# Kernel optimization log

Hardware: AMD Instinct MI355X
Metric: run time of the kernel (lower is better)

## Reference

```python
import jax, jax.numpy as jnp
import numpy as np

V = 32000   # vocab
E = 512     # hidden_size (d_model)
NH = 8      # num_heads
DH = E // NH
NL = 2      # num_layers
FF = 2048   # TransformerDecoderLayer default dim_feedforward
MAXLEN = 24 # cfg.max_length -> gen_len (no target given)
S, B = 48, 8
TRANS = 14
INIT = TRANS - 2            # tgt = transform[1:-1]
LF = INIT + MAXLEN - 1      # final tgt length after the loop
EPS = 1e-5
NEG = -1e9


def pos_encoding(length, d):
    pos = np.arange(length, dtype=np.float32)[:, None]
    div = np.exp(-np.log(10000.0) * np.arange(0, d, 2, dtype=np.float32) / d)
    pe = np.zeros((length, d), dtype=np.float32)
    pe[:, 0::2] = np.sin(pos * div)
    pe[:, 1::2] = np.cos(pos * div)
    return jnp.asarray(pe)


def setup_inputs() -> dict:
    key = jax.random.key(0)
    ks = jax.random.split(key, 12)
    s = 0.02
    return {
        "enc_outputs": jax.random.normal(ks[0], (S, B, E), jnp.float32),
        "transform": jax.random.randint(ks[1], (TRANS, B), 0, V),
        "tf_ratio": 0,
        "emb_table": jax.random.normal(ks[2], (V, E), jnp.float32) * s,
        "sa_w": jax.random.normal(ks[3], (NL, 3 * E, E), jnp.float32) * s,
        "sa_b": jnp.zeros((NL, 3 * E), jnp.float32),
        "sa_ow": jax.random.normal(ks[4], (NL, E, E), jnp.float32) * s,
        "sa_ob": jnp.zeros((NL, E), jnp.float32),
        "ca_w": jax.random.normal(ks[5], (NL, 3 * E, E), jnp.float32) * s,
        "ca_b": jnp.zeros((NL, 3 * E), jnp.float32),
        "ca_ow": jax.random.normal(ks[6], (NL, E, E), jnp.float32) * s,
        "ca_ob": jnp.zeros((NL, E), jnp.float32),
        "ff1_w": jax.random.normal(ks[7], (NL, FF, E), jnp.float32) * s,
        "ff1_b": jnp.zeros((NL, FF), jnp.float32),
        "ff2_w": jax.random.normal(ks[8], (NL, E, FF), jnp.float32) * s,
        "ff2_b": jnp.zeros((NL, E), jnp.float32),
        "ln_g": jnp.ones((NL, 3, E), jnp.float32),
        "ln_b": jnp.zeros((NL, 3, E), jnp.float32),
        "out_w": jax.random.normal(ks[9], (V, E), jnp.float32) * s,
        "out_b": jnp.zeros((V,), jnp.float32),
    }


def _ln(x, g, b):
    m = jnp.mean(x, -1, keepdims=True)
    v = jnp.mean((x - m) ** 2, -1, keepdims=True)
    return (x - m) * jax.lax.rsqrt(v + EPS) * g + b


def _mha(q_in, kv_in, w, b, ow, ob, mask):
    # q_in [Lq,B,E], kv_in [Lk,B,E]; PyTorch packed in_proj [3E,E]
    wq, wk, wv = jnp.split(w, 3, 0)
    bq, bk, bv = jnp.split(b, 3, 0)
    proj = lambda x, wm, bm: (x @ wm.T + bm).reshape(x.shape[0], x.shape[1], NH, DH)
    q, k, v = proj(q_in, wq, bq), proj(kv_in, wk, bk), proj(kv_in, wv, bv)
    sc = jnp.einsum('qbhd,kbhd->bhqk', q, k) / np.sqrt(DH).astype(np.float32)
    if mask is not None:
        sc = sc + mask
    a = jax.nn.softmax(sc, -1)
    o = jnp.einsum('bhqk,kbhd->qbhd', a, v).reshape(q_in.shape[0], q_in.shape[1], E)
    return o @ ow.T + ob


def _decoder(x, mem, mask, p):
    # post-norm TransformerDecoderLayer: self-attn -> cross-attn -> relu FFN
    for l in range(NL):
        x = _ln(x + _mha(x, x, p['sa_w'][l], p['sa_b'][l], p['sa_ow'][l], p['sa_ob'][l], mask),
                p['ln_g'][l, 0], p['ln_b'][l, 0])
        x = _ln(x + _mha(x, mem, p['ca_w'][l], p['ca_b'][l], p['ca_ow'][l], p['ca_ob'][l], None),
                p['ln_g'][l, 1], p['ln_b'][l, 1])
        h = jax.nn.relu(x @ p['ff1_w'][l].T + p['ff1_b'][l]) @ p['ff2_w'][l].T + p['ff2_b'][l]
        x = _ln(x + h, p['ln_g'][l, 2], p['ln_b'][l, 2])
    return x


def reference(enc_outputs, transform, tf_ratio, emb_table, sa_w, sa_b, sa_ow, sa_ob,
              ca_w, ca_b, ca_ow, ca_ob, ff1_w, ff1_b, ff2_w, ff2_b, ln_g, ln_b,
              out_w, out_b):
    # tf_ratio == 0 -> no teacher forcing; gen_len = max_length (no target attr)
    p = dict(sa_w=sa_w, sa_b=sa_b, sa_ow=sa_ow, sa_ob=sa_ob, ca_w=ca_w, ca_b=ca_b,
             ca_ow=ca_ow, ca_ob=ca_ob, ff1_w=ff1_w, ff1_b=ff1_b, ff2_w=ff2_w,
             ff2_b=ff2_b, ln_g=ln_g, ln_b=ln_b)
    pe = pos_encoding(MAXLEN, E)
    # causal mask over the fixed-size buffer; padded (future) slots cannot
    # influence valid positions, so full-buffer passes == torch prefix passes.
    mask = jnp.where(jnp.tril(jnp.ones((LF, LF), bool)), 0.0, NEG)
    tgt0 = emb_table[transform[1:-1]] + pe[:INIT][:, None, :]   # [INIT,B,E]
    buf = jnp.zeros((LF, B, E), jnp.float32).at[:INIT].set(tgt0)

    def step(buf, i):
        h = _decoder(buf, enc_outputs, mask, p)
        pos = INIT - 1 + i                        # last valid position
        pred = jnp.argmax(h[pos] @ out_w.T + out_b, axis=-1)   # [B]
        # torch re-embeds the single predicted token -> PE position 0
        emb = emb_table[pred] + pe[0]
        return buf.at[pos + 1].set(emb), None

    buf, _ = jax.lax.scan(step, buf, jnp.arange(MAXLEN - 1))
    h = _decoder(buf, enc_outputs, mask, p)       # final loop iteration's pass
    return h @ out_w.T + out_b                    # dec_outputs [LF,B,V]
```

## Files before the change

kernel.cpp:

```cpp
#include <hip/hip_runtime.h>
#include <hip/hip_bf16.h>
#include <math.h>

#define V    32000
#define E    512
#define NH   8
#define DH   64
#define NL   2
#define FF   2048
#define MAXLEN 24
#define S    48
#define B    8
#define TRANS 14
#define INIT 12
#define LF   35

#define NB   256
#define NT   1024

typedef float f4 __attribute__((ext_vector_type(4)));

__device__ inline float wsum(float v) {
#pragma unroll
  for (int off = 32; off; off >>= 1) v += __shfl_xor(v, off);
  return v;
}
__device__ inline float wmax(float v) {
#pragma unroll
  for (int off = 32; off; off >>= 1) v = fmaxf(v, __shfl_xor(v, off));
  return v;
}

__device__ inline void stc(float* p, float v) {
  __hip_atomic_store(p, v, __ATOMIC_RELAXED, __HIP_MEMORY_SCOPE_AGENT);
}
__device__ inline void stc8(float* p, float x, float y) {
  union { unsigned long long u; float f[2]; } c; c.f[0] = x; c.f[1] = y;
  __hip_atomic_store((unsigned long long*)p, c.u, __ATOMIC_RELAXED, __HIP_MEMORY_SCOPE_AGENT);
}
__device__ inline int ldci(const int* p) {
  return __hip_atomic_load(p, __ATOMIC_RELAXED, __HIP_MEMORY_SCOPE_AGENT);
}
__device__ inline void stci(int* p, int v) {
  __hip_atomic_store(p, v, __ATOMIC_RELAXED, __HIP_MEMORY_SCOPE_AGENT);
}

#define CMB(v, idx, ov, oi) do { if ((ov) > (v) || ((ov) == (v) && (oi) < (idx))) { (v) = (ov); (idx) = (oi); } } while (0)


__global__ void embed_init_k(const int* __restrict__ transform, const float* __restrict__ emb,
                             float* __restrict__ xbuf) {
  int t = blockIdx.x;
  int pos = t >> 3, b = t & 7;
  int tok = transform[(1 + pos) * B + b];
  for (int d = threadIdx.x; d < E; d += blockDim.x) {
    double div = exp(-log(10000.0) * (double)(d & ~1) / (double)E);
    double ang = (double)pos * div;
    float pe = (d & 1) ? (float)cos(ang) : (float)sin(ang);
    xbuf[(size_t)t * E + d] = emb[(size_t)tok * E + d] + pe;
  }
}

template <int K>
__global__ __launch_bounds__(256) void gemm_k(
    const float* __restrict__ x, const float* __restrict__ W, const float* __restrict__ bias,
    int ntok, int nout, int route, int relu,
    float* __restrict__ out0, float* __restrict__ out1, float* __restrict__ out2) {
  constexpr int K4 = K / 4;
  constexpr int J  = K / 256;
  __shared__ float4 xt[8][K4];
  const int tid = threadIdx.x;
  const int lane = tid & 63;
  const int o = blockIdx.x * 4 + (tid >> 6);

  float4 wr[J];
  if (o < nout) {
    const float4* Wr = (const float4*)(W + (size_t)o * K);
#pragma unroll
    for (int j = 0; j < J; ++j) wr[j] = Wr[lane + 64 * j];
  }

  const int ng = ntok >> 3;
  for (int g = 0; g < ng; ++g) {
    if (g) __syncthreads();
    const float4* xg = (const float4*)(x + (size_t)g * 8 * K);
    float4* xf = &xt[0][0];
    for (int i = tid; i < 8 * K4; i += 256) xf[i] = xg[i];
    __syncthreads();
    if (o < nout) {
      float acc[8] = {0, 0, 0, 0, 0, 0, 0, 0};
#pragma unroll
      for (int j = 0; j < J; ++j) {
        float4 w = wr[j];
#pragma unroll
        for (int tt = 0; tt < 8; ++tt) {
          float4 xv = xt[tt][lane + 64 * j];
          acc[tt] += w.x * xv.x + w.y * xv.y + w.z * xv.z + w.w * xv.w;
        }
      }
#pragma unroll
      for (int tt = 0; tt < 8; ++tt) acc[tt] = wsum(acc[tt]);
      if (lane == 0) {
        float bo = bias[o];
#pragma unroll
        for (int tt = 0; tt < 8; ++tt) {
          float v = acc[tt] + bo;
          if (relu) v = fmaxf(v, 0.f);
          int t = g * 8 + tt;
          if (route == 0) {
            out0[(size_t)t * nout + o] = v;
          } else if (route == 1) {
            if (o < E) out0[(size_t)t * E + o] = v;
            else if (o < 2 * E) out1[(size_t)t * E + (o - E)] = v;
            else out2[(size_t)t * E + (o - 2 * E)] = v;
          } else {
            if (o < E) out0[(size_t)t * E + o] = v;
            else out1[(size_t)t * E + (o - E)] = v;
          }
        }
      }
    }
  }
}

__global__ __launch_bounds__(256) void attn_k(
    const float* __restrict__ q, const float* __restrict__ Kc, const float* __restrict__ Vc,
    float* __restrict__ outp, int p0, int nq, int nk_fixed, int causal) {
  const int tid = threadIdx.x;
  const int lane = tid & 63;
  const int u = blockIdx.x * 4 + (tid >> 6);
  if (u >= nq * 64) return;
  const int qi = u >> 6;
  const int r = u & 63;
  const int b = r >> 3, h = r & 7;
  const int nk = causal ? (p0 + qi + 1) : nk_fixed;

  const size_t qoff = (size_t)(qi * B + b) * E + h * DH + lane;
  const float qv = q[qoff];

  float myscore = -INFINITY;
  for (int k = 0; k < nk; ++k) {
    float prod = qv * Kc[(size_t)(k * B + b) * E + h * DH + lane];
    prod = wsum(prod);
    if (lane == k) myscore = prod * 0.125f;
  }
  float m = wmax(myscore);
  float p = (lane < nk) ? expf(myscore - m) : 0.f;
  float denom = wsum(p);
  float a = p / denom;

  float oacc = 0.f;
  for (int k = 0; k < nk; ++k) {
    float ak = __shfl(a, k);
    oacc = fmaf(ak, Vc[(size_t)(k * B + b) * E + h * DH + lane], oacc);
  }
  outp[qoff] = oacc;
}

__global__ __launch_bounds__(256) void add_ln_k(
    const float* __restrict__ xa, const float* __restrict__ xb,
    const float* __restrict__ g, const float* __restrict__ beta,
    float* __restrict__ outp, int ntok) {
  const int tid = threadIdx.x, lane = tid & 63;
  const int t = blockIdx.x * 4 + (tid >> 6);
  if (t >= ntok) return;
  float v[8];
  float s = 0.f;
#pragma unroll
  for (int j = 0; j < 8; ++j) {
    int d = lane + 64 * j;
    v[j] = xa[(size_t)t * E + d] + xb[(size_t)t * E + d];
    s += v[j];
  }
  s = wsum(s);
  float mean = s * (1.f / 512.f);
  float d2 = 0.f;
#pragma unroll
  for (int j = 0; j < 8; ++j) { float dd = v[j] - mean; d2 += dd * dd; }
  d2 = wsum(d2);
  float inv = 1.f / sqrtf(d2 * (1.f / 512.f) + 1e-5f);
#pragma unroll
  for (int j = 0; j < 8; ++j) {
    int d = lane + 64 * j;
    outp[(size_t)t * E + d] = (v[j] - mean) * inv * g[d] + beta[d];
  }
}

#define B_QKV 0
#define B_OW  6144
#define B_CQ  8192
#define B_COW 10240
#define B_FF1 12288
#define B_FF2 20480
#define SW_TOT 28672
#define SLOTS_PER_STEP 23

__global__ __launch_bounds__(NT, 1) void decode_persist_k(
    const float* __restrict__ emb,
    const float* __restrict__ sa_w, const float* __restrict__ sa_b,
    const float* __restrict__ sa_ow, const float* __restrict__ sa_ob,
    const float* __restrict__ ca_w, const float* __restrict__ ca_b,
    const float* __restrict__ ca_ow, const float* __restrict__ ca_ob,
    const float* __restrict__ ff1_w, const float* __restrict__ ff1_b,
    const float* __restrict__ ff2_w, const float* __restrict__ ff2_b,
    const float* __restrict__ ln_g, const float* __restrict__ ln_b,
    const float* __restrict__ out_w, const float* __restrict__ out_b,
    float* __restrict__ kself, float* __restrict__ vself,
    const float* __restrict__ kcross, const float* __restrict__ vcross,
    float* __restrict__ arena, float* __restrict__ outp, int* __restrict__ bar) {
  __shared__ __align__(16) float s_w[SW_TOT];
  __shared__ __align__(16) float s_x[8 * E];
  __shared__ __align__(16) float s_raw[8 * E];
  __shared__ __align__(16) float s_q2[64];
  __shared__ __align__(16) float s_attw[64];
  __shared__ __align__(16) float s_part[4][64];
  __shared__ int   s_tok[8];
  __shared__ float s_pv[16][8];
  __shared__ int   s_pi[16][8];

  const int tid  = threadIdx.x;
  const int lane = tid & 63;
  const int wv   = tid >> 6;
  const int bid  = blockIdx.x;
  int gen = 0;

  auto slot = [&](int st, int s) -> float* {
    return arena + ((size_t)st * SLOTS_PER_STEP + s) * 4096;
  };

  auto gbar = [&]() {
    ++gen;
    __syncthreads();
    if (tid == 0)
      __hip_atomic_fetch_add(&bar[(bid & 31) * 32], 1, __ATOMIC_RELAXED, __HIP_MEMORY_SCOPE_AGENT);
    if (bid == 0 && wv == 0) {
      const int tgt = gen * 8;
      for (;;) {
        int c = (lane < 32) ? ldci(&bar[lane * 32]) : tgt;
        if (__all(c >= tgt)) break;
        __builtin_amdgcn_s_sleep(1);
      }
      if (lane == 0) stci(&bar[40 * 32], gen);
    }
    if (wv == 0) {
      while (ldci(&bar[40 * 32]) < gen) __builtin_amdgcn_s_sleep(2);
    }
    __syncthreads();
  };

  auto stage_raw = [&](const float* src) {
    const float4* s4 = (const float4*)src;
    float4* d4 = (float4*)s_raw;
    for (int k = tid; k < 1024; k += NT) d4[k] = s4[k];
    __syncthreads();
  };
  auto lnstage = [&](int lnidx) {
    if (wv < 8) {
      const float* gg = ln_g + (size_t)lnidx * E;
      const float* be = ln_b + (size_t)lnidx * E;
      float v[8]; float sum = 0.f;
#pragma unroll
      for (int j = 0; j < 8; ++j) {
        int d = lane + 64 * j;
        v[j] = s_x[wv * E + d] + s_raw[wv * E + d];
        sum += v[j];
      }
      sum = wsum(sum);
      float mean = sum * (1.f / 512.f);
      float d2 = 0.f;
#pragma unroll
      for (int j = 0; j < 8; ++j) { float dd = v[j] - mean; d2 += dd * dd; }
      d2 = wsum(d2);
      float inv = 1.f / sqrtf(d2 * (1.f / 512.f) + 1e-5f);
#pragma unroll
      for (int j = 0; j < 8; ++j) {
        int d = lane + 64 * j;
        s_x[wv * E + d] = (v[j] - mean) * inv * gg[d] + be[d];
      }
    }
    __syncthreads();
  };
  auto proj16 = [&](int wbase, const float* srcLDS, const float* biasp, float* dst) {
    int j = wv & 1, b = wv >> 1;
    int r = bid * 2 + j;
    const f4* wp = (const f4*)&s_w[wbase + j * 512];
    f4 w0 = wp[lane], w1 = wp[lane + 64];
    const f4* x4 = (const f4*)(srcLDS + b * E);
    f4 a = w0 * x4[lane] + w1 * x4[lane + 64];
    float acc = a.x + a.y + a.z + a.w;
    acc = wsum(acc);
    if (lane == 0) stc(&dst[b * E + r], acc + biasp[r]);
  };
  auto attn_stage = [&](const float* qsrc, const float* Kbase, const float* Vbase,
                        int nk, float* attdst) {
    const int b = bid >> 3, h = bid & 7;
    if (wv == 0) {
      s_q2[lane] = qsrc[b * E + h * DH + lane];
      float sc = -INFINITY;
      if (lane < nk) {
        const f4* Kr = (const f4*)(Kbase + ((size_t)lane * B + b) * E + h * DH);
        const f4* Qp = (const f4*)s_q2;
        float a0 = 0.f;
#pragma unroll
        for (int u = 0; u < 16; ++u) {
          f4 kv = Kr[u], qq = Qp[u];
          a0 += kv.x * qq.x + kv.y * qq.y + kv.z * qq.z + kv.w * qq.w;
        }
        sc = a0 * 0.125f;
      }
      float m = wmax(sc);
      float e = (lane < nk) ? expf(sc - m) : 0.f;
      float den = wsum(e);
      s_attw[lane] = e / den;
    }
    __syncthreads();
    if (wv < 4) {
      float o = 0.f;
      for (int k = wv; k < nk; k += 4)
        o = fmaf(s_attw[k], Vbase[((size_t)k * B + b) * E + h * DH + lane], o);
      s_part[wv][lane] = o;
    }
    __syncthreads();
    if (wv == 0)
      stc(&attdst[b * E + h * DH + lane],
          s_part[0][lane] + s_part[1][lane] + s_part[2][lane] + s_part[3][lane]);
  };

  {
    auto cprow = [&](const float* src, int dstf) {
      f4* d = (f4*)&s_w[dstf]; const f4* s = (const f4*)src;
      for (int k = tid; k < 128; k += NT) d[k] = s[k];
    };
    for (int l = 0; l < NL; ++l) {
      for (int j = 0; j < 6; ++j)
        cprow(sa_w + ((size_t)l * 1536 + bid * 6 + j) * E, B_QKV + (l * 6 + j) * 512);
      for (int j = 0; j < 2; ++j) {
        cprow(sa_ow + ((size_t)l * 512 + bid * 2 + j) * E, B_OW + (l * 2 + j) * 512);
        cprow(ca_w + ((size_t)l * 1536 + bid * 2 + j) * E, B_CQ + (l * 2 + j) * 512);
        cprow(ca_ow + ((size_t)l * 512 + bid * 2 + j) * E, B_COW + (l * 2 + j) * 512);
      }
      for (int j = 0; j < 8; ++j)
        cprow(ff1_w + ((size_t)l * FF + bid * 8 + j) * E, B_FF1 + (l * 8 + j) * 512);
    }
    const int lf2 = bid >> 7;
    for (int j = 0; j < 4; ++j) {
      f4* d = (f4*)&s_w[B_FF2 + j * 2048];
      const f4* s = (const f4*)(ff2_w + ((size_t)lf2 * 512 + (bid & 127) * 4 + j) * FF);
      for (int k = tid; k < 512; k += NT) d[k] = s[k];
    }
    __syncthreads();
  }

  for (int i = 0; i < MAXLEN - 1; ++i) {
    const int p = INIT + i;
    float* amax_o = slot(i, 0);

    {
      int bw = wv & 7;
      float v = -INFINITY; int ix = 0x7fffffff;
      if (i == 0) {
        const float2* row = (const float2*)(outp + ((size_t)(INIT - 1) * B + bw) * V);
        for (int jj = lane; jj < V / 2; jj += 64) {
          float2 t = row[jj];
          CMB(v, ix, t.x, 2 * jj);
          CMB(v, ix, t.y, 2 * jj + 1);
        }
      } else {
        const float2* ap = (const float2*)slot(i - 1, 0);
#pragma unroll
        for (int t = 0; t < 4; ++t) {
          int e = lane * 4 + t;
          float2 pr = ap[e * 8 + bw];
          CMB(v, ix, pr.x, (int)pr.y);
        }
      }
#pragma unroll
      for (int off = 1; off < 64; off <<= 1) {
        float ov = __shfl_xor(v, off); int oi = __shfl_xor(ix, off);
        CMB(v, ix, ov, oi);
      }
      if (lane == 0 && wv < 8) s_tok[bw] = ix;
      __syncthreads();
      int b = tid >> 7, d0 = (tid & 127) * 4;
      int tok = s_tok[b];
      float4 ev = *(const float4*)(emb + (size_t)tok * E + d0);
      s_x[b * E + d0]     = ev.x;
      s_x[b * E + d0 + 1] = ev.y + 1.0f;
      s_x[b * E + d0 + 2] = ev.z;
      s_x[b * E + d0 + 3] = ev.w + 1.0f;
      __syncthreads();
    }

    for (int l = 0; l < NL; ++l) {
      float* Lb    = slot(i, 1 + l * 11);
      float* q_s   = Lb;
      float* att_s = Lb + 4096;
      float* raw_s = Lb + 8192;
      float* q_c   = Lb + 12288;
      float* att_c = Lb + 16384;
      float* raw_c = Lb + 20480;
      float* hb    = Lb + 24576;
      float* yb    = Lb + 40960;

      if (wv < 12) {
        int j = wv >> 1, bg = (wv & 1) * 4;
        int r = bid * 6 + j, sec = r >> 9, off = r & 511;
        const f4* wp = (const f4*)&s_w[B_QKV + (l * 6 + j) * 512];
        f4 w0 = wp[lane], w1 = wp[lane + 64];
        float bias = sa_b[(size_t)l * 1536 + r];
        for (int b = bg; b < bg + 4; ++b) {
          const f4* x4 = (const f4*)&s_x[b * E];
          f4 a = w0 * x4[lane] + w1 * x4[lane + 64];
          float acc = a.x + a.y + a.z + a.w;
          acc = wsum(acc);
          if (lane == 0) {
            acc += bias;
            if (sec == 0) stc(&q_s[b * E + off], acc);
            else if (sec == 1) stc(&kself[((size_t)(l * LF + p) * B + b) * E + off], acc);
            else stc(&vself[((size_t)(l * LF + p) * B + b) * E + off], acc);
          }
        }
      }
      gbar();
      if (bid < 64)
        attn_stage(q_s, kself + (size_t)l * LF * B * E, vself + (size_t)l * LF * B * E,
                   p + 1, att_s);
      gbar();
      stage_raw(att_s);
      proj16(B_OW + l * 1024, s_raw, sa_ob + (size_t)l * E, raw_s);
      gbar();
      stage_raw(raw_s);
      lnstage(l * 3 + 0);
      proj16(B_CQ + l * 1024, s_x, ca_b + (size_t)l * 3 * E, q_c);
      gbar();
      if (bid < 64)
        attn_stage(q_c, kcross + (size_t)l * S * B * E, vcross + (size_t)l * S * B * E,
                   S, att_c);
      gbar();
      stage_raw(att_c);
      proj16(B_COW + l * 1024, s_raw, ca_ob + (size_t)l * E, raw_c);
      gbar();
      stage_raw(raw_c);
      lnstage(l * 3 + 1);
      {
        int j = wv >> 1, bg = (wv & 1) * 4;
        int r = bid * 8 + j;
        const f4* wp = (const f4*)&s_w[B_FF1 + (l * 8 + j) * 512];
        f4 w0 = wp[lane], w1 = wp[lane + 64];
        float bias = ff1_b[(size_t)l * FF + r];
        for (int b = bg; b < bg + 4; ++b) {
          const f4* x4 = (const f4*)&s_x[b * E];
          f4 a = w0 * x4[lane] + w1 * x4[lane + 64];
          float acc = a.x + a.y + a.z + a.w;
          acc = wsum(acc);
          if (lane == 0) stc(&hb[b * FF + r], fmaxf(acc + bias, 0.f));
        }
      }
      gbar();
      if ((bid >> 7) == l) {
        int b = wv >> 1, j0 = (wv & 1) * 2;
        int r0 = (bid & 127) * 4;
        const f4* h4 = (const f4*)(hb + b * FF);
        f4 hv[8];
#pragma unroll
        for (int j = 0; j < 8; ++j) hv[j] = h4[j * 64 + lane];
#pragma unroll
        for (int jr = 0; jr < 2; ++jr) {
          int rl = j0 + jr;
          const f4* wp = (const f4*)&s_w[B_FF2 + rl * 2048];
          float acc = 0.f;
#pragma unroll
          for (int j = 0; j < 8; ++j) {
            f4 w = wp[j * 64 + lane];
            acc += w.x * hv[j].x + w.y * hv[j].y + w.z * hv[j].z + w.w * hv[j].w;
          }
          acc = wsum(acc);
          if (lane == 0)
            stc(&yb[b * E + r0 + rl], acc + ff2_b[(size_t)l * 512 + r0 + rl]);
        }
      }
      gbar();
      stage_raw(yb);
      lnstage(l * 3 + 2);
    }

    {
      const int grp = lane >> 3, sub = lane & 7;
      const int idx = wv * 8 + grp;
      const bool valid = idx < 125;
      const int r = bid * 125 + idx;
      float acc[8] = {0, 0, 0, 0, 0, 0, 0, 0};
      if (valid) {
        const f4* wrow = (const f4*)(out_w + (size_t)r * E);
#pragma unroll
        for (int half = 0; half < 2; ++half) {
          f4 w8[8];
#pragma unroll
          for (int j = 0; j < 8; ++j) w8[j] = wrow[(half * 8 + j) * 8 + sub];
#pragma unroll
          for (int b = 0; b < 8; ++b) {
            const f4* x4 = (const f4*)&s_x[b * E];
            float a = 0.f;
#pragma unroll
            for (int j = 0; j < 8; ++j) {
              f4 xx = x4[(half * 8 + j) * 8 + sub];
              a += w8[j].x * xx.x + w8[j].y * xx.y + w8[j].z * xx.z + w8[j].w * xx.w;
            }
            acc[b] += a;
          }
        }
#pragma unroll
        for (int b = 0; b < 8; ++b) {
          acc[b] += __shfl_xor(acc[b], 1);
          acc[b] += __shfl_xor(acc[b], 2);
          acc[b] += __shfl_xor(acc[b], 4);
        }
        if (sub == 0) {
          float bo = out_b[r];
#pragma unroll
          for (int b = 0; b < 8; ++b) {
            acc[b] += bo;
            outp[((size_t)p * B + b) * V + r] = acc[b];
          }
        }
      }
#pragma unroll
      for (int b = 0; b < 8; ++b) {
        float v = (valid && sub == 0) ? acc[b] : -INFINITY;
        int ix = (valid && sub == 0) ? r : 0x7fffffff;
#pragma unroll
        for (int off = 1; off < 64; off <<= 1) {
          float ov = __shfl_xor(v, off); int oi = __shfl_xor(ix, off);
          CMB(v, ix, ov, oi);
        }
        if (lane == 0) { s_pv[wv][b] = v; s_pi[wv][b] = ix; }
      }
      __syncthreads();
      if (wv == 0) {
        int b = lane & 7, w2 = lane >> 3;
        float v = s_pv[w2][b]; int ix = s_pi[w2][b];
        float v2 = s_pv[w2 + 8][b]; int ix2 = s_pi[w2 + 8][b];
        CMB(v, ix, v2, ix2);
#pragma unroll
        for (int off = 8; off < 64; off <<= 1) {
          float ov = __shfl_xor(v, off); int oi = __shfl_xor(ix, off);
          CMB(v, ix, ov, oi);
        }
        if (lane < 8) stc8(&amax_o[(size_t)(bid * 8 + lane) * 2], v, (float)ix);
      }
    }
    gbar();
  }
}

extern "C" void kernel_launch(void* const* d_in, const int* in_sizes, int n_in,
                              void* d_out, int out_size, void* d_ws, size_t ws_size,
                              hipStream_t stream) {
  const float* enc       = (const float*)d_in[0];
  const int*   transform = (const int*)d_in[1];
  const float* emb       = (const float*)d_in[3];
  const float* sa_w  = (const float*)d_in[4];
  const float* sa_b  = (const float*)d_in[5];
  const float* sa_ow = (const float*)d_in[6];
  const float* sa_ob = (const float*)d_in[7];
  const float* ca_w  = (const float*)d_in[8];
  const float* ca_b  = (const float*)d_in[9];
  const float* ca_ow = (const float*)d_in[10];
  const float* ca_ob = (const float*)d_in[11];
  const float* ff1_w = (const float*)d_in[12];
  const float* ff1_b = (const float*)d_in[13];
  const float* ff2_w = (const float*)d_in[14];
  const float* ff2_b = (const float*)d_in[15];
  const float* ln_g  = (const float*)d_in[16];
  const float* ln_b  = (const float*)d_in[17];
  const float* out_w = (const float*)d_in[18];
  const float* out_b = (const float*)d_in[19];
  float* out = (float*)d_out;

  const size_t SELF_SZ  = (size_t)LF * B * E;
  const size_t CROSS_SZ = (size_t)S * B * E;
  const size_t ARENA_SZ = (size_t)(MAXLEN - 1) * SLOTS_PER_STEP * 4096;
  float* ws     = (float*)d_ws;
  float* xbuf   = ws;
  float* kself  = xbuf + (size_t)INIT * B * E;
  float* vself  = kself + NL * SELF_SZ;
  float* kcross = vself + NL * SELF_SZ;
  float* vcross = kcross + NL * CROSS_SZ;
  float* arena  = vcross + NL * CROSS_SZ;
  int*   bar    = (int*)(arena + ARENA_SZ);
  float* act1   = (float*)(bar + 64 * 32);
  float* act2   = act1 + 96 * E;
  float* act3   = act2 + 96 * E;
  float* ffb    = act3 + 96 * E;

  hipMemsetAsync(bar, 0, 64 * 32 * 4, stream);

  embed_init_k<<<INIT * B, 128, 0, stream>>>(transform, emb, xbuf);

  for (int l = 0; l < NL; ++l) {
    gemm_k<E><<<(2 * E) / 4, 256, 0, stream>>>(
        enc, ca_w + ((size_t)l * 3 * E + E) * E, ca_b + (size_t)l * 3 * E + E,
        S * B, 2 * E, 2, 0, kcross + l * CROSS_SZ, vcross + l * CROSS_SZ, nullptr);
  }

  {
    const int p0 = 0, nq = INIT, ntok = nq * B;
    const float* xin = xbuf;
    for (int l = 0; l < NL; ++l) {
      const float* x = (l == 0) ? xin : act1;
      gemm_k<E><<<(3 * E) / 4, 256, 0, stream>>>(
          x, sa_w + (size_t)l * 3 * E * E, sa_b + (size_t)l * 3 * E, ntok, 3 * E, 1, 0,
          act2, kself + l * SELF_SZ, vself + l * SELF_SZ);
      attn_k<<<nq * 16, 256, 0, stream>>>(act2, kself + l * SELF_SZ, vself + l * SELF_SZ,
                                          act3, p0, nq, 0, 1);
      gemm_k<E><<<E / 4, 256, 0, stream>>>(
          act3, sa_ow + (size_t)l * E * E, sa_ob + (size_t)l * E, ntok, E, 0, 0, act2, nullptr, nullptr);
      add_ln_k<<<(ntok + 3) / 4, 256, 0, stream>>>(
          x, act2, ln_g + (size_t)l * 3 * E, ln_b + (size_t)l * 3 * E, act1, ntok);
      gemm_k<E><<<E / 4, 256, 0, stream>>>(
          act1, ca_w + (size_t)l * 3 * E * E, ca_b + (size_t)l * 3 * E, ntok, E, 0, 0, act2, nullptr, nullptr);
      attn_k<<<nq * 16, 256, 0, stream>>>(act2, kcross + l * CROSS_SZ, vcross + l * CROSS_SZ,
                                          act3, p0, nq, S, 0);
      gemm_k<E><<<E / 4, 256, 0, stream>>>(
          act3, ca_ow + (size_t)l * E * E, ca_ob + (size_t)l * E, ntok, E, 0, 0, act2, nullptr, nullptr);
      add_ln_k<<<(ntok + 3) / 4, 256, 0, stream>>>(
          act1, act2, ln_g + (size_t)l * 3 * E + E, ln_b + (size_t)l * 3 * E + E, act1, ntok);
      gemm_k<E><<<FF / 4, 256, 0, stream>>>(
          act1, ff1_w + (size_t)l * FF * E, ff1_b + (size_t)l * FF, ntok, FF, 0, 1, ffb, nullptr, nullptr);
      gemm_k<FF><<<E / 4, 256, 0, stream>>>(
          ffb, ff2_w + (size_t)l * E * FF, ff2_b + (size_t)l * E, ntok, E, 0, 0, act2, nullptr, nullptr);
      add_ln_k<<<(ntok + 3) / 4, 256, 0, stream>>>(
          act1, act2, ln_g + (size_t)l * 3 * E + 2 * E, ln_b + (size_t)l * 3 * E + 2 * E, act1, ntok);
    }
    gemm_k<E><<<V / 4, 256, 0, stream>>>(
        act1, out_w, out_b, ntok, V, 0, 0, out, nullptr, nullptr);
  }

  decode_persist_k<<<NB, NT, 0, stream>>>(
      emb, sa_w, sa_b, sa_ow, sa_ob, ca_w, ca_b, ca_ow, ca_ob,
      ff1_w, ff1_b, ff2_w, ff2_b, ln_g, ln_b, out_w, out_b,
      kself, vself, kcross, vcross, arena, out, bar);
}
```

Before: 4.996 ms.

## Replace centralized grid barrier with per-stage producer flag waits

Replaces the counter-based grid barrier, which had block 0 aggregate counts and then broadcast a release generation, with per-stage, per-block flags. Consumers poll only the flags of the blocks that produced the data they need: 64 blocks after attention, 128 after FF2, 256 otherwise. Each block polls its flags starting at a staggered offset, and the end-of-step barrier becomes a flag wait at the start of the next step. This removes the two-hop barrier latency and lets blocks proceed as soon as their producers finish, at the cost of more polling traffic (each block reads up to 256 flags) and a longer sleep between polls.

```diff
diff --git a/kernel.cpp b/kernel.cpp
--- a/kernel.cpp
+++ b/kernel.cpp
@@ -194,6 +194,7 @@
 #define B_FF2 20480
 #define SW_TOT 28672
 #define SLOTS_PER_STEP 23
+#define NSTAGE 17
 
 __global__ __launch_bounds__(NT, 1) void decode_persist_k(
     const float* __restrict__ emb,
@@ -222,28 +223,27 @@
   const int lane = tid & 63;
   const int wv   = tid >> 6;
   const int bid  = blockIdx.x;
-  int gen = 0;
 
   auto slot = [&](int st, int s) -> float* {
     return arena + ((size_t)st * SLOTS_PER_STEP + s) * 4096;
   };
 
-  auto gbar = [&]() {
-    ++gen;
-    __syncthreads();
-    if (tid == 0)
-      __hip_atomic_fetch_add(&bar[(bid & 31) * 32], 1, __ATOMIC_RELAXED, __HIP_MEMORY_SCOPE_AGENT);
-    if (bid == 0 && wv == 0) {
-      const int tgt = gen * 8;
+  auto flg = [&](int s, int j) -> int* { return &bar[(s * 256 + j) * 16]; };
+
+  auto set_flag = [&](int s, int tgt, bool producer) {
+    __syncthreads();
+    if (producer && tid == 0) stci(flg(s, bid), tgt);
+  };
+  auto wait_flags = [&](int s, int base, int count, int tgt) {
+    if (wv == 0) {
+      const int m = count - 1;
       for (;;) {
-        int c = (lane < 32) ? ldci(&bar[lane * 32]) : tgt;
-        if (__all(c >= tgt)) break;
-        __builtin_amdgcn_s_sleep(1);
-      }
-      if (lane == 0) stci(&bar[40 * 32], gen);
-    }
-    if (wv == 0) {
-      while (ldci(&bar[40 * 32]) < gen) __builtin_amdgcn_s_sleep(2);
+        bool ok = true;
+        for (int f = lane; f < count; f += 64)
+          ok &= (ldci(flg(s, base + ((f + bid) & m))) >= tgt);
+        if (__all(ok)) break;
+        __builtin_amdgcn_s_sleep(12);
+      }
     }
     __syncthreads();
   };
@@ -353,8 +353,10 @@
 
   for (int i = 0; i < MAXLEN - 1; ++i) {
     const int p = INIT + i;
+    const int tgt = i + 1;
     float* amax_o = slot(i, 0);
 
+    if (i > 0) wait_flags(16, 0, 256, i);
     {
       int bw = wv & 7;
       float v = -INFINITY; int ix = 0x7fffffff;
@@ -392,6 +394,7 @@
     }
 
     for (int l = 0; l < NL; ++l) {
+      const int sb = l * 8;
       float* Lb    = slot(i, 1 + l * 11);
       float* q_s   = Lb;
       float* att_s = Lb + 4096;
@@ -421,25 +424,31 @@
           }
         }
       }
-      gbar();
+      set_flag(sb + 0, tgt, true);
+      wait_flags(sb + 0, 0, 256, tgt);
       if (bid < 64)
         attn_stage(q_s, kself + (size_t)l * LF * B * E, vself + (size_t)l * LF * B * E,
                    p + 1, att_s);
-      gbar();
+      set_flag(sb + 1, tgt, bid < 64);
+      wait_flags(sb + 1, 0, 64, tgt);
       stage_raw(att_s);
       proj16(B_OW + l * 1024, s_raw, sa_ob + (size_t)l * E, raw_s);
-      gbar();
+      set_flag(sb + 2, tgt, true);
+      wait_flags(sb + 2, 0, 256, tgt);
       stage_raw(raw_s);
       lnstage(l * 3 + 0);
       proj16(B_CQ + l * 1024, s_x, ca_b + (size_t)l * 3 * E, q_c);
-      gbar();
+      set_flag(sb + 3, tgt, true);
+      wait_flags(sb + 3, 0, 256, tgt);
       if (bid < 64)
         attn_stage(q_c, kcross + (size_t)l * S * B * E, vcross + (size_t)l * S * B * E,
                    S, att_c);
-      gbar();
+      set_flag(sb + 4, tgt, bid < 64);
+      wait_flags(sb + 4, 0, 64, tgt);
       stage_raw(att_c);
       proj16(B_COW + l * 1024, s_raw, ca_ob + (size_t)l * E, raw_c);
-      gbar();
+      set_flag(sb + 5, tgt, true);
+      wait_flags(sb + 5, 0, 256, tgt);
       stage_raw(raw_c);
       lnstage(l * 3 + 1);
       {
@@ -456,7 +465,8 @@
           if (lane == 0) stc(&hb[b * FF + r], fmaxf(acc + bias, 0.f));
         }
       }
-      gbar();
+      set_flag(sb + 6, tgt, true);
+      wait_flags(sb + 6, 0, 256, tgt);
       if ((bid >> 7) == l) {
         int b = wv >> 1, j0 = (wv & 1) * 2;
         int r0 = (bid & 127) * 4;
@@ -479,7 +489,8 @@
             stc(&yb[b * E + r0 + rl], acc + ff2_b[(size_t)l * 512 + r0 + rl]);
         }
       }
-      gbar();
+      set_flag(sb + 7, tgt, (bid >> 7) == l);
+      wait_flags(sb + 7, l * 128, 128, tgt);
       stage_raw(yb);
       lnstage(l * 3 + 2);
     }
@@ -549,7 +560,7 @@
         if (lane < 8) stc8(&amax_o[(size_t)(bid * 8 + lane) * 2], v, (float)ix);
       }
     }
-    gbar();
+    set_flag(16, tgt, true);
   }
 }
 
@@ -580,6 +591,7 @@
   const size_t SELF_SZ  = (size_t)LF * B * E;
   const size_t CROSS_SZ = (size_t)S * B * E;
   const size_t ARENA_SZ = (size_t)(MAXLEN - 1) * SLOTS_PER_STEP * 4096;
+  const size_t FLAG_SZ  = (size_t)NSTAGE * 256 * 16;
   float* ws     = (float*)d_ws;
   float* xbuf   = ws;
   float* kself  = xbuf + (size_t)INIT * B * E;
@@ -588,12 +600,12 @@
   float* vcross = kcross + NL * CROSS_SZ;
   float* arena  = vcross + NL * CROSS_SZ;
   int*   bar    = (int*)(arena + ARENA_SZ);
-  float* act1   = (float*)(bar + 64 * 32);
+  float* act1   = (float*)(bar + FLAG_SZ);
   float* act2   = act1 + 96 * E;
   float* act3   = act2 + 96 * E;
   float* ffb    = act3 + 96 * E;
 
-  hipMemsetAsync(bar, 0, 64 * 32 * 4, stream);
+  hipMemsetAsync(bar, 0, FLAG_SZ * 4, stream);
 
   embed_init_k<<<INIT * B, 128, 0, stream>>>(transform, emb, xbuf);
 
```

New measurement: 5.071 ms. Within noise of the previous version (+1.5%).
